# Performance work log

Measured on AMD Instinct MI355X. Metric: run time of the kernel, lower is better.

## Reference

```python
import jax, jax.numpy as jnp
import numpy as np

EPS = 1e-12  # matches torch F.normalize default eps
TEMP = 0.1


def _gram(x):
    # L2-normalize rows; for unit vectors 1 - 0.5*||xi-xj||^2 == xi . xj
    n = x / jnp.maximum(jnp.linalg.norm(x, axis=-1, keepdims=True), EPS)
    return n @ n.T  # [N, N]


def setup_inputs() -> dict:
    key = jax.random.key(0)
    k1, k2, k3, k4 = jax.random.split(key, 4)
    N, D = 4096, 512
    return {
        "fm_rgb": jax.random.normal(k1, (N, D), dtype=jnp.float32),
        "fm_depth": jax.random.normal(k2, (N, D), dtype=jnp.float32),
        "fm_ir": jax.random.normal(k3, (N, D), dtype=jnp.float32),
        "fm_t": jax.random.normal(k4, (N, D), dtype=jnp.float32),
    }


def reference(fm_rgb, fm_depth, fm_ir, fm_t):
    G_rgb = _gram(fm_rgb)
    G_depth = _gram(fm_depth)
    G_ir = _gram(fm_ir)
    G_t = _gram(fm_t)
    inv_t = 1.0 / TEMP
    loss_rgb = jnp.mean((G_t * inv_t - G_rgb * inv_t) ** 2)
    loss_depth = jnp.mean((G_t * inv_t - G_depth * inv_t) ** 2)
    loss_ir = jnp.mean((G_t * inv_t - G_ir * inv_t) ** 2)
    return loss_rgb + loss_depth + loss_ir
```

## Files before the change

kernel.cpp:

```cpp
#include <hip/hip_runtime.h>
#include <hip/hip_bf16.h>


typedef __attribute__((ext_vector_type(4))) float floatx4;
typedef __attribute__((ext_vector_type(2))) long long llx2;
typedef __attribute__((ext_vector_type(8))) int intx8;

#define N_ROWS 4096
#define DDIM   512
#define LOSS_SCALE 9.094947017729282e-11f

__device__ __forceinline__ const float* sel_mod(int mod, const float* a,
                                                const float* b, const float* c,
                                                const float* d) {
  return mod == 0 ? a : mod == 1 ? b : mod == 2 ? c : d;
}

__device__ __forceinline__ float bfr(float x) {
  __hip_bfloat16 h = __float2bfloat16(x);
  unsigned short u = *(unsigned short*)&h;
  return __uint_as_float(((unsigned int)u) << 16);
}

__global__ __launch_bounds__(512) void preprocess_kernel(
    const float* __restrict__ in0, const float* __restrict__ in1,
    const float* __restrict__ in2, const float* __restrict__ in3,
    unsigned char* __restrict__ nT8, float* __restrict__ out) {
  int mod = blockIdx.y;
  int k0 = blockIdx.x * 64;
  const float* X = sel_mod(mod, in0, in1, in2, in3) + (size_t)k0 * DDIM;

  if (blockIdx.x == 0 && blockIdx.y == 0 && threadIdx.x == 0)
    out[0] = 0.f;

  __shared__ float rsc[64];
  __shared__ unsigned int t8[512 * 17];

  int t = threadIdx.x;
  int a = t >> 5;
  int bg = t & 31;

  float4 v[4][4];
#pragma unroll
  for (int q = 0; q < 4; ++q)
#pragma unroll
    for (int p = 0; p < 4; ++p)
      v[q][p] = ((const float4*)(X + (size_t)(4 * a + q) * DDIM + p * 128))[bg];

  float ss[4];
#pragma unroll
  for (int q = 0; q < 4; ++q) {
    float acc = 0.f;
#pragma unroll
    for (int p = 0; p < 4; ++p) {
      float4 u = v[q][p];
      acc += u.x * u.x + u.y * u.y + u.z * u.z + u.w * u.w;
    }
    ss[q] = acc;
  }
#pragma unroll
  for (int off = 16; off > 0; off >>= 1)
#pragma unroll
    for (int q = 0; q < 4; ++q) ss[q] += __shfl_down(ss[q], off, 32);
  if (bg == 0) {
#pragma unroll
    for (int q = 0; q < 4; ++q)
      rsc[4 * a + q] = 16.0f / fmaxf(sqrtf(ss[q]), 1e-12f);
  }
  __syncthreads();

  float sc[4];
#pragma unroll
  for (int q = 0; q < 4; ++q) sc[q] = rsc[4 * a + q];

#pragma unroll
  for (int p = 0; p < 4; ++p)
#pragma unroll
    for (int j = 0; j < 4; ++j) {
      float f0 = bfr(((const float*)&v[0][p])[j] * sc[0]);
      float f1 = bfr(((const float*)&v[1][p])[j] * sc[1]);
      float f2 = bfr(((const float*)&v[2][p])[j] * sc[2]);
      float f3 = bfr(((const float*)&v[3][p])[j] * sc[3]);
      unsigned int pk = __builtin_amdgcn_cvt_pk_fp8_f32(f0, f1, 0, 0);
      pk = __builtin_amdgcn_cvt_pk_fp8_f32(f2, f3, pk, 1);
      t8[(p * 128 + bg * 4 + j) * 17 + a] = pk;
    }
  __syncthreads();

  size_t rbase = (size_t)(mod * 64 + blockIdx.x) * 32768;
#pragma unroll
  for (int it = 0; it < 4; ++it) {
    int idx = it * 512 + t;
    int col = idx >> 2;
    int g = idx & 3;
    uint4 o;
    o.x = t8[col * 17 + g * 4 + 0];
    o.y = t8[col * 17 + g * 4 + 1];
    o.z = t8[col * 17 + g * 4 + 2];
    o.w = t8[col * 17 + g * 4 + 3];
    *(uint4*)(nT8 + rbase + (size_t)idx * 16) = o;
  }
}

__device__ __forceinline__ void stage_half(
    const unsigned char* __restrict__ mbase, int cbase, int k0,
    unsigned char* ls, int lane) {
  int rr = lane >> 3;
  int s = lane & 7;
  int kb0 = k0 >> 6;
#pragma unroll
  for (int c = 0; c < 8; ++c) {
    int row = c * 8 + rr;
    int gc = s ^ ((row >> 1) & 7);
    const unsigned char* g =
        mbase + ((size_t)(kb0 + (gc >> 2)) * 512 + cbase + row) * 64 +
        (gc & 3) * 16;
    __builtin_amdgcn_global_load_lds(
        (__attribute__((address_space(1))) void*)(void*)g,
        (__attribute__((address_space(3))) void*)(void*)&ls[c * 1024],
        16, 0, 0);
  }
}

__device__ __forceinline__ void compute_w(const unsigned char* ls,
                                          floatx4 acc[4][2], int wn, int lm,
                                          int lq) {
  intx8 A8[4], B8[2];
#pragma unroll
  for (int mi = 0; mi < 4; ++mi) {
    int row = mi * 16 + lm;
    int sw = (row >> 1) & 7;
    *(llx2*)&A8[mi] = *(const llx2*)&ls[row * 128 + ((lq * 2) ^ sw) * 16];
    *((llx2*)&A8[mi] + 1) =
        *(const llx2*)&ls[row * 128 + ((lq * 2 + 1) ^ sw) * 16];
  }
#pragma unroll
  for (int ni = 0; ni < 2; ++ni) {
    int row = wn + ni * 16 + lm;
    int sw = (row >> 1) & 7;
    *(llx2*)&B8[ni] =
        *(const llx2*)&ls[8192 + row * 128 + ((lq * 2) ^ sw) * 16];
    *((llx2*)&B8[ni] + 1) =
        *(const llx2*)&ls[8192 + row * 128 + ((lq * 2 + 1) ^ sw) * 16];
  }
  __builtin_amdgcn_s_setprio(1);
#pragma unroll
  for (int mi = 0; mi < 4; ++mi)
#pragma unroll
    for (int ni = 0; ni < 2; ++ni)
      acc[mi][ni] = __builtin_amdgcn_mfma_scale_f32_16x16x128_f8f6f4(
          A8[mi], B8[ni], acc[mi][ni], 0, 0,
          0, 0x7F, 0, 0x7F);
  __builtin_amdgcn_s_setprio(0);
}

__global__ __launch_bounds__(128) void gram_frob_kernel(
    const unsigned char* __restrict__ nT8, float* __restrict__ out) {
  __shared__ __align__(16) unsigned char ls[5][16384];

  int bx = blockIdx.x;
  int job = (bx & 7) * 42 + (bx >> 3);

  int rem = job, ti = 7, tj = 7;
  for (int i = 0; i < 8; ++i) {
    int rowlen = 7 + 10 * (7 - i);
    if (rem < rowlen) {
      if (rem < 7) {
        ti = i; tj = i;
      } else {
        int r2 = rem - 7;
        ti = i; tj = i + 1 + r2 / 10;
        rem = r2 % 10;
      }
      break;
    }
    rem -= rowlen;
  }

  int pa_, pb_, a0, b0;
  float wgt;
  if (ti == tj) {
    if (rem < 4) { pa_ = pb_ = rem; wgt = (rem == 3) ? 3.f : 1.f; }
    else         { pa_ = 3; pb_ = rem - 4; wgt = -2.f; }
    a0 = ti * 64; b0 = ti * 64;
  } else {
    if (rem < 4) {
      pa_ = pb_ = rem; wgt = (rem == 3) ? 6.f : 2.f;
      a0 = ti * 64; b0 = tj * 64;
    } else {
      int k = rem - 4;
      pa_ = 3; pb_ = k >> 1; wgt = -2.f;
      if (k & 1) { a0 = tj * 64; b0 = ti * 64; }
      else       { a0 = ti * 64; b0 = tj * 64; }
    }
  }

  const unsigned char* Abase = nT8 + (size_t)pa_ * 2097152;
  const unsigned char* Bbase = nT8 + (size_t)pb_ * 2097152;

  int t = threadIdx.x;
  int w = t >> 6;
  int lane = t & 63;
  int lm = lane & 15;
  int lq = lane >> 4;
  int wn = w * 32;
  const unsigned char* mbase = (w == 0) ? Abase : Bbase;
  int cb = (w == 0) ? a0 : b0;
  int soff = w * 8192;

  floatx4 zero = {0.f, 0.f, 0.f, 0.f};
  floatx4 acc[4][2];
#pragma unroll
  for (int mi = 0; mi < 4; ++mi)
#pragma unroll
    for (int ni = 0; ni < 2; ++ni) acc[mi][ni] = zero;

  unsigned char* p0 = ls[0] + soff;
  unsigned char* p1 = ls[1] + soff;
  unsigned char* p2 = ls[2] + soff;
  unsigned char* p3 = ls[3] + soff;
  unsigned char* p4 = ls[4] + soff;
  stage_half(mbase, cb, 0, p0, lane);
  stage_half(mbase, cb, 128, p1, lane);
  stage_half(mbase, cb, 256, p2, lane);
  stage_half(mbase, cb, 384, p3, lane);
  for (int i = 0; i < 28; ++i) {
    asm volatile("s_waitcnt vmcnt(24)" ::: "memory");
    __builtin_amdgcn_sched_barrier(0);
    __builtin_amdgcn_s_barrier();
    stage_half(mbase, cb, (i + 4) * 128, p4, lane);
    compute_w(p0 - soff, acc, wn, lm, lq);
    unsigned char* tmp = p0; p0 = p1; p1 = p2; p2 = p3; p3 = p4; p4 = tmp;
  }
  asm volatile("s_waitcnt vmcnt(24)" ::: "memory");
  __builtin_amdgcn_sched_barrier(0);
  __builtin_amdgcn_s_barrier();
  compute_w(p0 - soff, acc, wn, lm, lq);
  asm volatile("s_waitcnt vmcnt(16)" ::: "memory");
  __builtin_amdgcn_sched_barrier(0);
  __builtin_amdgcn_s_barrier();
  compute_w(p1 - soff, acc, wn, lm, lq);
  asm volatile("s_waitcnt vmcnt(8)" ::: "memory");
  __builtin_amdgcn_sched_barrier(0);
  __builtin_amdgcn_s_barrier();
  compute_w(p2 - soff, acc, wn, lm, lq);
  asm volatile("s_waitcnt vmcnt(0)" ::: "memory");
  __builtin_amdgcn_sched_barrier(0);
  __builtin_amdgcn_s_barrier();
  compute_w(p3 - soff, acc, wn, lm, lq);

  float s = 0.f;
#pragma unroll
  for (int mi = 0; mi < 4; ++mi)
#pragma unroll
    for (int ni = 0; ni < 2; ++ni)
#pragma unroll
      for (int r = 0; r < 4; ++r) {
        float v = acc[mi][ni][r];
        s += v * v;
      }
#pragma unroll
  for (int off = 32; off > 0; off >>= 1) s += __shfl_down(s, off, 64);
  if (lane == 0)
    atomicAdd(out, wgt * LOSS_SCALE * s);
}

extern "C" void kernel_launch(void* const* d_in, const int* in_sizes, int n_in,
                              void* d_out, int out_size, void* d_ws, size_t ws_size,
                              hipStream_t stream) {
  const float* in_rgb   = (const float*)d_in[0];
  const float* in_depth = (const float*)d_in[1];
  const float* in_ir    = (const float*)d_in[2];
  const float* in_t     = (const float*)d_in[3];

  unsigned char* nT8 = (unsigned char*)d_ws;

  preprocess_kernel<<<dim3(64, 4), 512, 0, stream>>>(
      in_rgb, in_depth, in_ir, in_t, nT8, (float*)d_out);
  gram_frob_kernel<<<dim3(336), 128, 0, stream>>>(nT8, (float*)d_out);
}
```

Before: 101.8 us.

## Drop LDS staging; load MFMA fragments directly from global with 32x32 single-wave tiles

Replaces the five-stage LDS pipeline (two waves staging 64x64 tiles via global_load_lds) with single-wave blocks that each compute a 32x32 quadrant, loading fp8 MFMA fragments straight from global memory into registers with a two-stage register double buffer. The grid grows from 336 to 1344 blocks to spread more work across CUs and remove barrier and LDS overhead. In exchange, the reuse each tile gets from one load drops and global/L2 traffic rises, and latency hiding now relies on register prefetch and occupancy.

```diff
diff --git a/kernel.cpp b/kernel.cpp
--- a/kernel.cpp
+++ b/kernel.cpp
@@ -102,64 +102,21 @@
   }
 }
 
-__device__ __forceinline__ void stage_half(
-    const unsigned char* __restrict__ mbase, int cbase, int k0,
-    unsigned char* ls, int lane) {
-  int rr = lane >> 3;
-  int s = lane & 7;
-  int kb0 = k0 >> 6;
-#pragma unroll
-  for (int c = 0; c < 8; ++c) {
-    int row = c * 8 + rr;
-    int gc = s ^ ((row >> 1) & 7);
-    const unsigned char* g =
-        mbase + ((size_t)(kb0 + (gc >> 2)) * 512 + cbase + row) * 64 +
-        (gc & 3) * 16;
-    __builtin_amdgcn_global_load_lds(
-        (__attribute__((address_space(1))) void*)(void*)g,
-        (__attribute__((address_space(3))) void*)(void*)&ls[c * 1024],
-        16, 0, 0);
-  }
-}
-
-__device__ __forceinline__ void compute_w(const unsigned char* ls,
-                                          floatx4 acc[4][2], int wn, int lm,
-                                          int lq) {
-  intx8 A8[4], B8[2];
-#pragma unroll
-  for (int mi = 0; mi < 4; ++mi) {
-    int row = mi * 16 + lm;
-    int sw = (row >> 1) & 7;
-    *(llx2*)&A8[mi] = *(const llx2*)&ls[row * 128 + ((lq * 2) ^ sw) * 16];
-    *((llx2*)&A8[mi] + 1) =
-        *(const llx2*)&ls[row * 128 + ((lq * 2 + 1) ^ sw) * 16];
-  }
-#pragma unroll
-  for (int ni = 0; ni < 2; ++ni) {
-    int row = wn + ni * 16 + lm;
-    int sw = (row >> 1) & 7;
-    *(llx2*)&B8[ni] =
-        *(const llx2*)&ls[8192 + row * 128 + ((lq * 2) ^ sw) * 16];
-    *((llx2*)&B8[ni] + 1) =
-        *(const llx2*)&ls[8192 + row * 128 + ((lq * 2 + 1) ^ sw) * 16];
-  }
-  __builtin_amdgcn_s_setprio(1);
-#pragma unroll
-  for (int mi = 0; mi < 4; ++mi)
-#pragma unroll
-    for (int ni = 0; ni < 2; ++ni)
-      acc[mi][ni] = __builtin_amdgcn_mfma_scale_f32_16x16x128_f8f6f4(
-          A8[mi], B8[ni], acc[mi][ni], 0, 0,
-          0, 0x7F, 0, 0x7F);
-  __builtin_amdgcn_s_setprio(0);
-}
-
-__global__ __launch_bounds__(128) void gram_frob_kernel(
+__device__ __forceinline__ intx8 ldfrag(const unsigned char* __restrict__ p) {
+  intx8 r;
+  *(llx2*)&r = *(const llx2*)p;
+  *((llx2*)&r + 1) = *(const llx2*)(p + 16);
+  return r;
+}
+
+__global__ __launch_bounds__(64) void gram_frob_kernel(
     const unsigned char* __restrict__ nT8, float* __restrict__ out) {
-  __shared__ __align__(16) unsigned char ls[5][16384];
-
   int bx = blockIdx.x;
-  int job = (bx & 7) * 42 + (bx >> 3);
+  int u = (bx & 7) * 168 + (bx >> 3);
+  int job = u >> 2;
+  int quad = u & 3;
+  int mh = quad >> 1;
+  int nh = quad & 1;
 
   int rem = job, ti = 7, tj = 7;
   for (int i = 0; i < 8; ++i) {
@@ -195,63 +152,62 @@
     }
   }
 
-  const unsigned char* Abase = nT8 + (size_t)pa_ * 2097152;
-  const unsigned char* Bbase = nT8 + (size_t)pb_ * 2097152;
-
-  int t = threadIdx.x;
-  int w = t >> 6;
-  int lane = t & 63;
+  int lane = threadIdx.x;
   int lm = lane & 15;
   int lq = lane >> 4;
-  int wn = w * 32;
-  const unsigned char* mbase = (w == 0) ? Abase : Bbase;
-  int cb = (w == 0) ? a0 : b0;
-  int soff = w * 8192;
+
+  size_t lkb = ((size_t)(lq >> 1) * 512 + lm) * 64 + (size_t)(lq & 1) * 32;
+  const unsigned char* pA0 =
+      nT8 + (size_t)pa_ * 2097152 + lkb + (size_t)(a0 + 32 * mh) * 64;
+  const unsigned char* pA1 = pA0 + 16 * 64;
+  const unsigned char* pB0 =
+      nT8 + (size_t)pb_ * 2097152 + lkb + (size_t)(b0 + 32 * nh) * 64;
+  const unsigned char* pB1 = pB0 + 16 * 64;
+#define CHUNK_STRIDE 65536
 
   floatx4 zero = {0.f, 0.f, 0.f, 0.f};
-  floatx4 acc[4][2];
-#pragma unroll
-  for (int mi = 0; mi < 4; ++mi)
-#pragma unroll
-    for (int ni = 0; ni < 2; ++ni) acc[mi][ni] = zero;
-
-  unsigned char* p0 = ls[0] + soff;
-  unsigned char* p1 = ls[1] + soff;
-  unsigned char* p2 = ls[2] + soff;
-  unsigned char* p3 = ls[3] + soff;
-  unsigned char* p4 = ls[4] + soff;
-  stage_half(mbase, cb, 0, p0, lane);
-  stage_half(mbase, cb, 128, p1, lane);
-  stage_half(mbase, cb, 256, p2, lane);
-  stage_half(mbase, cb, 384, p3, lane);
-  for (int i = 0; i < 28; ++i) {
-    asm volatile("s_waitcnt vmcnt(24)" ::: "memory");
-    __builtin_amdgcn_sched_barrier(0);
-    __builtin_amdgcn_s_barrier();
-    stage_half(mbase, cb, (i + 4) * 128, p4, lane);
-    compute_w(p0 - soff, acc, wn, lm, lq);
-    unsigned char* tmp = p0; p0 = p1; p1 = p2; p2 = p3; p3 = p4; p4 = tmp;
-  }
-  asm volatile("s_waitcnt vmcnt(24)" ::: "memory");
-  __builtin_amdgcn_sched_barrier(0);
-  __builtin_amdgcn_s_barrier();
-  compute_w(p0 - soff, acc, wn, lm, lq);
-  asm volatile("s_waitcnt vmcnt(16)" ::: "memory");
-  __builtin_amdgcn_sched_barrier(0);
-  __builtin_amdgcn_s_barrier();
-  compute_w(p1 - soff, acc, wn, lm, lq);
-  asm volatile("s_waitcnt vmcnt(8)" ::: "memory");
-  __builtin_amdgcn_sched_barrier(0);
-  __builtin_amdgcn_s_barrier();
-  compute_w(p2 - soff, acc, wn, lm, lq);
-  asm volatile("s_waitcnt vmcnt(0)" ::: "memory");
-  __builtin_amdgcn_sched_barrier(0);
-  __builtin_amdgcn_s_barrier();
-  compute_w(p3 - soff, acc, wn, lm, lq);
+  floatx4 acc[2][2];
+  acc[0][0] = zero; acc[0][1] = zero; acc[1][0] = zero; acc[1][1] = zero;
+
+#define MFMA4(AR, BR)                                                        \
+  do {                                                                       \
+    __builtin_amdgcn_s_setprio(1);                                           \
+    acc[0][0] = __builtin_amdgcn_mfma_scale_f32_16x16x128_f8f6f4(            \
+        AR[0], BR[0], acc[0][0], 0, 0, 0, 0x7F, 0, 0x7F);                    \
+    acc[0][1] = __builtin_amdgcn_mfma_scale_f32_16x16x128_f8f6f4(            \
+        AR[0], BR[1], acc[0][1], 0, 0, 0, 0x7F, 0, 0x7F);                    \
+    acc[1][0] = __builtin_amdgcn_mfma_scale_f32_16x16x128_f8f6f4(            \
+        AR[1], BR[0], acc[1][0], 0, 0, 0, 0x7F, 0, 0x7F);                    \
+    acc[1][1] = __builtin_amdgcn_mfma_scale_f32_16x16x128_f8f6f4(            \
+        AR[1], BR[1], acc[1][1], 0, 0, 0, 0x7F, 0, 0x7F);                    \
+    __builtin_amdgcn_s_setprio(0);                                           \
+  } while (0)
+
+  intx8 ae[2], be[2], ao[2], bo[2];
+  ae[0] = ldfrag(pA0); ae[1] = ldfrag(pA1);
+  be[0] = ldfrag(pB0); be[1] = ldfrag(pB1);
+  for (int ch = 0; ch < 30; ch += 2) {
+    pA0 += CHUNK_STRIDE; pA1 += CHUNK_STRIDE;
+    pB0 += CHUNK_STRIDE; pB1 += CHUNK_STRIDE;
+    ao[0] = ldfrag(pA0); ao[1] = ldfrag(pA1);
+    bo[0] = ldfrag(pB0); bo[1] = ldfrag(pB1);
+    MFMA4(ae, be);
+    pA0 += CHUNK_STRIDE; pA1 += CHUNK_STRIDE;
+    pB0 += CHUNK_STRIDE; pB1 += CHUNK_STRIDE;
+    ae[0] = ldfrag(pA0); ae[1] = ldfrag(pA1);
+    be[0] = ldfrag(pB0); be[1] = ldfrag(pB1);
+    MFMA4(ao, bo);
+  }
+  pA0 += CHUNK_STRIDE; pA1 += CHUNK_STRIDE;
+  pB0 += CHUNK_STRIDE; pB1 += CHUNK_STRIDE;
+  ao[0] = ldfrag(pA0); ao[1] = ldfrag(pA1);
+  bo[0] = ldfrag(pB0); bo[1] = ldfrag(pB1);
+  MFMA4(ae, be);
+  MFMA4(ao, bo);
 
   float s = 0.f;
 #pragma unroll
-  for (int mi = 0; mi < 4; ++mi)
+  for (int mi = 0; mi < 2; ++mi)
 #pragma unroll
     for (int ni = 0; ni < 2; ++ni)
 #pragma unroll
@@ -277,5 +233,5 @@
 
   preprocess_kernel<<<dim3(64, 4), 512, 0, stream>>>(
       in_rgb, in_depth, in_ir, in_t, nT8, (float*)d_out);
-  gram_frob_kernel<<<dim3(336), 128, 0, stream>>>(nT8, (float*)d_out);
-}
+  gram_frob_kernel<<<dim3(1344), 64, 0, stream>>>(nT8, (float*)d_out);
+}
```

Result: slower. 117.7 us (+15.6%).
